# Optimization experiments

Measured on AMD Instinct MI355X. Metric: run time of the kernel, lower is better.

Reference implementation:

```python
import jax, jax.numpy as jnp
import numpy as np
from jax import lax

B, BERT_DIM, Z_DIM, ODE_UNITS, T_MAX = 4096, 768, 64, 128, 512
LN_EPS = 1e-5

def _glorot(key, shape):
    fan_in, fan_out = shape[0], shape[1]
    lim = float(np.sqrt(6.0 / (fan_in + fan_out)))
    return jax.random.uniform(key, shape, jnp.float32, -lim, lim)

def setup_inputs() -> dict:
    key = jax.random.key(0)
    ks = jax.random.split(key, 16)
    inp = {
        'bert_emb': jax.random.normal(ks[0], (B, BERT_DIM), jnp.float32),
        'times': jax.random.uniform(ks[1], (B, T_MAX), jnp.float32),
        'seq_lens': jax.random.randint(ks[2], (B,), 0, T_MAX).astype(jnp.int64),
        'eps': jax.random.normal(ks[3], (B, Z_DIM), jnp.float32),
        # bert_proj: Linear(768->64) + LayerNorm(64)
        'proj_W': _glorot(ks[4], (BERT_DIM, Z_DIM)),
        'proj_b': jnp.zeros((Z_DIM,), jnp.float32),
        'ln_g': jnp.ones((Z_DIM,), jnp.float32),
        'ln_b': jnp.zeros((Z_DIM,), jnp.float32),
        # DiffusionAug
        'log_noise_std': jnp.float32(-2.0),
        'den_W1': _glorot(ks[5], (Z_DIM, 2 * Z_DIM)),
        'den_b1': jnp.zeros((2 * Z_DIM,), jnp.float32),
        'den_W2': _glorot(ks[6], (2 * Z_DIM, Z_DIM)),
        'den_b2': jnp.zeros((Z_DIM,), jnp.float32),
        # ODEFunc: Linear->Tanh->Linear->Tanh->Linear (xavier_uniform, zero bias)
        'ode_W1': _glorot(ks[7], (Z_DIM, ODE_UNITS)),
        'ode_b1': jnp.zeros((ODE_UNITS,), jnp.float32),
        'ode_W2': _glorot(ks[8], (ODE_UNITS, ODE_UNITS)),
        'ode_b2': jnp.zeros((ODE_UNITS,), jnp.float32),
        'ode_W3': _glorot(ks[9], (ODE_UNITS, Z_DIM)),
        'ode_b3': jnp.zeros((Z_DIM,), jnp.float32),
        # dec_head: Linear(64->2)
        'dec_W': _glorot(ks[10], (Z_DIM, 2)),
        'dec_b': jnp.zeros((2,), jnp.float32),
    }
    return inp

def reference(bert_emb, times, seq_lens, eps, proj_W, proj_b, ln_g, ln_b,
              log_noise_std, den_W1, den_b1, den_W2, den_b2,
              ode_W1, ode_b1, ode_W2, ode_b2, ode_W3, ode_b3, dec_W, dec_b):
    T = times.shape[1]
    # bert_proj: Linear + LayerNorm (dropout = identity in eval)
    h = bert_emb @ proj_W + proj_b
    mu = jnp.mean(h, axis=-1, keepdims=True)
    var = jnp.var(h, axis=-1, keepdims=True)
    z_clean = (h - mu) * lax.rsqrt(var + LN_EPS) * ln_g + ln_b
    # DiffusionAug: noise + denoise MLP, MSE to detached clean latent
    sigma = jax.nn.softplus(log_noise_std)
    z_noisy = z_clean + sigma * eps
    z_aug = jax.nn.silu(z_noisy @ den_W1 + den_b1) @ den_W2 + den_b2
    diff_loss = jnp.mean((z_aug - lax.stop_gradient(z_clean)) ** 2)
    # Euler ODE integration: z <- z + dt * f(z), T sequential steps
    dt = jnp.float32(1.0 / max(T, 1))
    def step(z, _):
        f = jnp.tanh(jnp.tanh(z @ ode_W1 + ode_b1) @ ode_W2 + ode_b2) @ ode_W3 + ode_b3
        z_new = z + dt * f
        return z_new, z_new
    _, zs = lax.scan(step, z_aug, None, length=T)  # zs: (T, B, z)
    traj = jnp.concatenate([z_aug[:, None, :], jnp.swapaxes(zs, 0, 1)], axis=1)  # (B, T+1, z)
    out = traj @ dec_W + dec_b  # (B, T+1, 2)
    pred_delta = out[:, :, 0]
    stop_logits = out[:, :, 1]
    return (pred_delta, stop_logits, diff_loss)
```

## Files before the change

kernel.cpp:

```cpp
#include <hip/hip_runtime.h>
#include <stdint.h>

#define NB 4096
#define NT 512
#define OT 513
#define TOTE (NB*OT)
#define LOSSOFF (2*TOTE)

typedef float  f32x4 __attribute__((ext_vector_type(4)));
typedef __fp16 f16x8 __attribute__((ext_vector_type(8)));
typedef __fp16 f16x2 __attribute__((ext_vector_type(2)));

#define MFMA(A,B,C) __builtin_amdgcn_mfma_f32_16x16x32_f16((A),(B),(C),0,0,0)

__device__ __forceinline__ void wg_barrier() {
  asm volatile("s_waitcnt lgkmcnt(0)\n\ts_barrier" ::: "memory");
}

__device__ __forceinline__ float fast_tanh(float x) {
  float e = __builtin_amdgcn_exp2f(x * 2.8853900817779268f);
  return __builtin_fmaf(-2.0f, __builtin_amdgcn_rcpf(1.0f + e), 1.0f);
}
__device__ __forceinline__ float fast_silu(float x) {
  float e = __builtin_amdgcn_exp2f(x * -1.4426950408889634f);
  return x * __builtin_amdgcn_rcpf(1.0f + e);
}
__device__ __forceinline__ uint32_t pk2(float a, float b) {
  union { f16x2 h; uint32_t u; } c;
  c.h = __builtin_amdgcn_cvt_pkrtz(a, b);
  return c.u;
}
__device__ __forceinline__ f16x8 pack8(f32x4 a, f32x4 b) {
  union { f16x8 v; f16x2 h[4]; } u;
  u.h[0] = __builtin_amdgcn_cvt_pkrtz(a.x, a.y);
  u.h[1] = __builtin_amdgcn_cvt_pkrtz(a.z, a.w);
  u.h[2] = __builtin_amdgcn_cvt_pkrtz(b.x, b.y);
  u.h[3] = __builtin_amdgcn_cvt_pkrtz(b.z, b.w);
  return u.v;
}

#define WS_WPAK (1u<<20)
#define WS_UBUF ((1u<<20) + (256u<<10))
#define WS_CBUF ((1u<<20) + (384u<<10))

__global__ void compose_kernel(const float* __restrict__ oW1, const float* __restrict__ oW3,
                               const float* __restrict__ ob3, const float* __restrict__ dW,
                               float* __restrict__ Ubuf, float* __restrict__ cbuf,
                               float* __restrict__ dout) {
  int g = blockIdx.x, tid = threadIdx.x;
  if (g < 72) {
    int e = g * 256 + tid;
    int i = e / 144, j = e - i * 144;
    float s = 0.f;
    if (j < 128) {
      #pragma unroll 4
      for (int k = 0; k < 64; k++) s = __builtin_fmaf(oW3[i * 64 + k], oW1[k * 128 + j], s);
    } else if (j < 130) {
      int cc = j - 128;
      for (int k = 0; k < 64; k++) s = __builtin_fmaf(oW3[i * 64 + k], dW[k * 2 + cc], s);
    }
    Ubuf[i * 144 + j] = s;
  } else {
    if (tid < 144) {
      float s = 0.f;
      if (tid < 128) {
        for (int k = 0; k < 64; k++) s = __builtin_fmaf(ob3[k], oW1[k * 128 + tid], s);
      } else if (tid < 130) {
        int cc = tid - 128;
        for (int k = 0; k < 64; k++) s = __builtin_fmaf(ob3[k], dW[k * 2 + cc], s);
      }
      cbuf[tid] = s;
    }
    if (tid == 255) dout[LOSSOFF] = 0.0f;
  }
}

__global__ void pack_kernel(const float* __restrict__ oW1, const float* __restrict__ oW2,
                            const float* __restrict__ dW,  const float* __restrict__ dW1,
                            const float* __restrict__ dW2, const float* __restrict__ pW,
                            const float* __restrict__ Ubuf, char* __restrict__ wdst) {
  int g = blockIdx.x * 256 + threadIdx.x;
  int fid = g >> 6, lane = g & 63;
  if (fid >= 228 || (fid >= 50 && fid < 64)) return;
  int m4 = lane & 15;
  if (fid >= 48 && fid < 50) {
    int kt = fid - 48;
    int k0 = kt * 32 + (lane >> 4) * 8;
    f16x8 out;
    #pragma unroll
    for (int j = 0; j < 8; j++) out[j] = (m4 < 2) ? (__fp16)dW[(k0 + j) * 2 + m4] : (__fp16)0.f;
    *(f16x8*)(wdst + (size_t)(fid * 64 + lane) * 16) = out;
    return;
  }
  const float* src; int Kt, M, base;
  if      (fid < 16)  { src = oW1;  Kt = 2;  M = 128; base = 0;   }
  else if (fid < 48)  { src = oW2;  Kt = 4;  M = 128; base = 16;  }
  else if (fid < 80)  { src = dW1;  Kt = 2;  M = 128; base = 64;  }
  else if (fid < 96)  { src = dW2;  Kt = 4;  M = 64;  base = 80;  }
  else if (fid < 192) { src = pW;   Kt = 24; M = 64;  base = 96;  }
  else                { src = Ubuf; Kt = 4;  M = 144; base = 192; }
  int local = fid - base;
  int mt = local / Kt, kt = local % Kt;
  int m  = mt * 16 + m4;
  int k0 = kt * 32 + (lane >> 4) * 8;
  f16x8 out;
  #pragma unroll
  for (int j = 0; j < 8; j++) out[j] = (__fp16)src[(size_t)(k0 + j) * M + m];
  *(f16x8*)(wdst + (size_t)(fid * 64 + lane) * 16) = out;
}

__global__ __launch_bounds__(512, 2) void prologue_kernel(
    const float* __restrict__ bert, const float* __restrict__ eps,
    const float* __restrict__ projb, const float* __restrict__ lng,
    const float* __restrict__ lnb,  const float* __restrict__ lns,
    const float* __restrict__ db1,  const float* __restrict__ db2,
    const char* __restrict__ wpack, float* __restrict__ wsz,
    float* __restrict__ dout) {
  __shared__ __attribute__((aligned(16))) char sZ[16 * 128];
  __shared__ __attribute__((aligned(16))) char sH[16 * 256];
  __shared__ f32x4  sScr[4 * 64];
  __shared__ float2 sMV[64];
  __shared__ float  sLsum[4];

  const int tid  = threadIdx.x;
  const int wave = tid >> 6, lane = tid & 63;
  const int q = lane >> 4, b = lane & 15;
  const int bg = blockIdx.x * 16 + b;
  const int b7 = b & 7;
  const f16x8* wp = (const f16x8*)wpack;
  const int u0 = wave * 16 + q * 4;

  const int zr0 = b * 128 + ((q    ) ^ b7) * 16;
  const int zr1 = b * 128 + ((q + 4) ^ b7) * 16;
  int hr[4];
  #pragma unroll
  for (int s = 0; s < 4; s++) hr[s] = b * 256 + ((4 * s + q) ^ b7) * 16;
  const int hw = b * 256 + (((2 * wave + (q >> 1)) ^ b7) * 16) + (q & 1) * 8;
  const int zw = b * 128 + (((2 * (wave & 3) + (q >> 1)) ^ b7) * 16) + (q & 1) * 8;

  const int mt = wave & 3, kh = wave >> 2;
  f32x4 hA = {0,0,0,0}, hB = {0,0,0,0};
  #pragma unroll 4
  for (int i = 0; i < 12; i++) {
    int kt = kh * 12 + i;
    f16x8 af = wp[(size_t)(96 + mt * 24 + kt) * 64 + lane];
    const float* bp = bert + (size_t)bg * 768 + kt * 32 + q * 8;
    f32x4 f0 = *(const f32x4*)bp;
    f32x4 f1 = *(const f32x4*)(bp + 4);
    f16x8 bf = pack8(f0, f1);
    if (i & 1) hB = MFMA(af, bf, hB); else hA = MFMA(af, bf, hA);
  }
  f32x4 hacc = hA + hB;
  if (wave >= 4) sScr[(wave - 4) * 64 + lane] = hacc;
  __syncthreads();

  f32x4 h = {0,0,0,0}, zc = {0,0,0,0};
  if (wave < 4) {
    h = hacc + sScr[wave * 64 + lane];
    h.x += projb[u0 + 0]; h.y += projb[u0 + 1];
    h.z += projb[u0 + 2]; h.w += projb[u0 + 3];
    float s1 = h.x + h.y + h.z + h.w;
    float s2 = h.x*h.x + h.y*h.y + h.z*h.z + h.w*h.w;
    s1 += __shfl_xor(s1, 16); s1 += __shfl_xor(s1, 32);
    s2 += __shfl_xor(s2, 16); s2 += __shfl_xor(s2, 32);
    if (q == 0) sMV[wave * 16 + b] = make_float2(s1, s2);
  }
  __syncthreads();
  if (wave < 4) {
    float t1 = 0.f, t2 = 0.f;
    #pragma unroll
    for (int w2 = 0; w2 < 4; w2++) { float2 m = sMV[w2 * 16 + b]; t1 += m.x; t2 += m.y; }
    float mu  = t1 * (1.0f / 64.0f);
    float var = t2 * (1.0f / 64.0f) - mu * mu;
    float rs  = rsqrtf(var + 1e-5f);
    float sigma = logf(1.0f + expf(lns[0]));
    f32x4 e = *(const f32x4*)(eps + (size_t)bg * 64 + u0);
    zc.x = __builtin_fmaf((h.x - mu) * rs, lng[u0+0], lnb[u0+0]);
    zc.y = __builtin_fmaf((h.y - mu) * rs, lng[u0+1], lnb[u0+1]);
    zc.z = __builtin_fmaf((h.z - mu) * rs, lng[u0+2], lnb[u0+2]);
    zc.w = __builtin_fmaf((h.w - mu) * rs, lng[u0+3], lnb[u0+3]);
    f32x4 zn = zc + sigma * e;
    *(uint2*)(sZ + zw) = make_uint2(pk2(zn.x, zn.y), pk2(zn.z, zn.w));
  }
  __syncthreads();
  {
    f16x8 w0 = wp[(size_t)(64 + wave * 2 + 0) * 64 + lane];
    f16x8 w1 = wp[(size_t)(64 + wave * 2 + 1) * 64 + lane];
    f16x8 bz0 = *(const f16x8*)(sZ + zr0);
    f16x8 bz1 = *(const f16x8*)(sZ + zr1);
    f32x4 bias = { db1[u0+0], db1[u0+1], db1[u0+2], db1[u0+3] };
    f32x4 acc = MFMA(w0, bz0, bias);
    acc = MFMA(w1, bz1, acc);
    *(uint2*)(sH + hw) = make_uint2(pk2(fast_silu(acc.x), fast_silu(acc.y)),
                                    pk2(fast_silu(acc.z), fast_silu(acc.w)));
  }
  __syncthreads();
  if (wave < 4) {
    f16x8 w0 = wp[(size_t)(80 + wave * 4 + 0) * 64 + lane];
    f16x8 w1 = wp[(size_t)(80 + wave * 4 + 1) * 64 + lane];
    f16x8 w2 = wp[(size_t)(80 + wave * 4 + 2) * 64 + lane];
    f16x8 w3 = wp[(size_t)(80 + wave * 4 + 3) * 64 + lane];
    f16x8 g0 = *(const f16x8*)(sH + hr[0]);
    f16x8 g1 = *(const f16x8*)(sH + hr[1]);
    f16x8 g2 = *(const f16x8*)(sH + hr[2]);
    f16x8 g3 = *(const f16x8*)(sH + hr[3]);
    f32x4 bias = { db2[u0+0], db2[u0+1], db2[u0+2], db2[u0+3] };
    const f32x4 z4 = {0,0,0,0};
    f32x4 aA = MFMA(w0, g0, bias); aA = MFMA(w1, g1, aA);
    f32x4 aB = MFMA(w2, g2, z4);   aB = MFMA(w3, g3, aB);
    f32x4 za = aA + aB;
    *(f32x4*)(wsz + (size_t)bg * 64 + u0) = za;
    f32x4 d = za - zc;
    float sl = d.x*d.x + d.y*d.y + d.z*d.z + d.w*d.w;
    const int offs[6] = {1, 2, 4, 8, 16, 32};
    #pragma unroll
    for (int i = 0; i < 6; i++) sl += __shfl_xor(sl, offs[i]);
    if (lane == 0) sLsum[wave] = sl;
  }
  __syncthreads();
  if (tid == 0)
    atomicAdd(dout + LOSSOFF,
              (sLsum[0] + sLsum[1] + sLsum[2] + sLsum[3]) * (1.0f / 262144.0f));
}

__global__ __launch_bounds__(512, 1) void ode_kernel(
    const float* __restrict__ wsz, const char* __restrict__ wpack,
    const float* __restrict__ ob1, const float* __restrict__ cbuf,
    const float* __restrict__ ob2, const float* __restrict__ decb,
    float* __restrict__ dout) {
  __shared__ __attribute__((aligned(16))) char sH1[4096];
  __shared__ __attribute__((aligned(16))) char sH2[4096];

  const int tid  = threadIdx.x;
  const int wave = tid >> 6, lane = tid & 63;
  const int q = lane >> 4, b = lane & 15;
  const f16x8* wp = (const f16x8*)wpack;
  const float dtc = 1.0f / 512.0f;
  const f32x4 zero4 = {0,0,0,0};

  int rd[4];
  #pragma unroll
  for (int kt = 0; kt < 4; kt++) rd[kt] = b * 256 + (((kt * 4 + q) ^ b) * 16);
  const int wr = b * 256 + (((wave * 2 + (q >> 1)) ^ b) * 16) + (q & 1) * 8;

  f16x8 w2f[4], uf[4], uf8[4];
  #pragma unroll
  for (int kt = 0; kt < 4; kt++) {
    w2f[kt] = wp[(size_t)(16  + wave * 4 + kt) * 64 + lane];
    uf [kt] = wp[(size_t)(192 + wave * 4 + kt) * 64 + lane];
  }
  if (wave == 7) {
    #pragma unroll
    for (int kt = 0; kt < 4; kt++)
      uf8[kt] = wp[(size_t)(192 + 32 + kt) * 64 + lane];
  }
  const f32x4 b2f = *(const f32x4*)(ob2  + wave * 16 + q * 4);
  const f32x4 cw  = *(const f32x4*)(cbuf + wave * 16 + q * 4);
  const f32x4 c8  = *(const f32x4*)(cbuf + 128 + q * 4);

  const int bg = blockIdx.x * 16 + b;
  const float* zrow = wsz + (size_t)bg * 64;
  f32x4 z0a = *(const f32x4*)(zrow + q * 8);
  f32x4 z0b = *(const f32x4*)(zrow + q * 8 + 4);
  f32x4 z1a = *(const f32x4*)(zrow + 32 + q * 8);
  f32x4 z1b = *(const f32x4*)(zrow + 32 + q * 8 + 4);
  f16x8 zf0 = pack8(z0a, z0b);
  f16x8 zf1 = pack8(z1a, z1b);

  f32x4 b1v = *(const f32x4*)(ob1 + wave * 16 + q * 4);
  f32x4 G = MFMA(wp[(size_t)(wave * 2 + 0) * 64 + lane], zf0, b1v);
  G = MFMA(wp[(size_t)(wave * 2 + 1) * 64 + lane], zf1, G);
  *(uint2*)(sH1 + wr) = make_uint2(pk2(fast_tanh(G.x), fast_tanh(G.y)),
                                   pk2(fast_tanh(G.z), fast_tanh(G.w)));

  f32x4 Gd = zero4;
  float* const outp_p = dout + (size_t)bg * OT;
  float* const outp_s = dout + (size_t)TOTE + (size_t)bg * OT;
  if (wave == 7) {
    f32x4 b1d = zero4;
    if (q == 0) { b1d.x = decb[0]; b1d.y = decb[1]; }
    Gd = MFMA(wp[(size_t)48 * 64 + lane], zf0, b1d);
    Gd = MFMA(wp[(size_t)49 * 64 + lane], zf1, Gd);
    if (q == 0) { outp_p[0] = Gd.x; outp_s[0] = Gd.y; }
  }
  wg_barrier();

  #pragma unroll 1
  for (int t = 0; t < NT; ++t) {
    f16x8 p0 = *(const f16x8*)(sH1 + rd[0]);
    f16x8 p1 = *(const f16x8*)(sH1 + rd[1]);
    f16x8 p2 = *(const f16x8*)(sH1 + rd[2]);
    f16x8 p3 = *(const f16x8*)(sH1 + rd[3]);
    f32x4 a  = MFMA(w2f[0], p0, b2f);
    a  = MFMA(w2f[1], p1, a);
    f32x4 a2 = MFMA(w2f[2], p2, zero4);
    a2 = MFMA(w2f[3], p3, a2);
    f32x4 hv = a + a2;
    *(uint2*)(sH2 + wr) = make_uint2(pk2(fast_tanh(hv.x), fast_tanh(hv.y)),
                                     pk2(fast_tanh(hv.z), fast_tanh(hv.w)));
    wg_barrier();

    f16x8 g0 = *(const f16x8*)(sH2 + rd[0]);
    f16x8 g1 = *(const f16x8*)(sH2 + rd[1]);
    f16x8 g2 = *(const f16x8*)(sH2 + rd[2]);
    f16x8 g3 = *(const f16x8*)(sH2 + rd[3]);
    f32x4 d  = MFMA(uf[0], g0, cw);
    d  = MFMA(uf[1], g1, d);
    f32x4 d2 = MFMA(uf[2], g2, zero4);
    d2 = MFMA(uf[3], g3, d2);
    G.x = __builtin_fmaf(dtc, d.x + d2.x, G.x);
    G.y = __builtin_fmaf(dtc, d.y + d2.y, G.y);
    G.z = __builtin_fmaf(dtc, d.z + d2.z, G.z);
    G.w = __builtin_fmaf(dtc, d.w + d2.w, G.w);
    *(uint2*)(sH1 + wr) = make_uint2(pk2(fast_tanh(G.x), fast_tanh(G.y)),
                                     pk2(fast_tanh(G.z), fast_tanh(G.w)));
    if (wave == 7) {
      f32x4 e  = MFMA(uf8[0], g0, c8);
      e  = MFMA(uf8[1], g1, e);
      f32x4 e2 = MFMA(uf8[2], g2, zero4);
      e2 = MFMA(uf8[3], g3, e2);
      Gd.x = __builtin_fmaf(dtc, e.x + e2.x, Gd.x);
      Gd.y = __builtin_fmaf(dtc, e.y + e2.y, Gd.y);
      if (q == 0) { outp_p[t + 1] = Gd.x; outp_s[t + 1] = Gd.y; }
    }
    wg_barrier();
  }
}

extern "C" void kernel_launch(void* const* d_in, const int* in_sizes, int n_in,
                              void* d_out, int out_size, void* d_ws, size_t ws_size,
                              hipStream_t stream) {
  const float* bert  = (const float*)d_in[0];
  const float* eps   = (const float*)d_in[3];
  const float* projW = (const float*)d_in[4];
  const float* projb = (const float*)d_in[5];
  const float* lng   = (const float*)d_in[6];
  const float* lnb   = (const float*)d_in[7];
  const float* lns   = (const float*)d_in[8];
  const float* denW1 = (const float*)d_in[9];
  const float* denb1 = (const float*)d_in[10];
  const float* denW2 = (const float*)d_in[11];
  const float* denb2 = (const float*)d_in[12];
  const float* odeW1 = (const float*)d_in[13];
  const float* odeb1 = (const float*)d_in[14];
  const float* odeW2 = (const float*)d_in[15];
  const float* odeb2 = (const float*)d_in[16];
  const float* odeW3 = (const float*)d_in[17];
  const float* odeb3 = (const float*)d_in[18];
  const float* decW  = (const float*)d_in[19];
  const float* decb  = (const float*)d_in[20];
  float* dout = (float*)d_out;

  float* wsz  = (float*)d_ws;
  char*  wpak = (char*)d_ws + WS_WPAK;
  float* Ubuf = (float*)((char*)d_ws + WS_UBUF);
  float* cbuf = (float*)((char*)d_ws + WS_CBUF);

  compose_kernel<<<73, 256, 0, stream>>>(odeW1, odeW3, odeb3, decW, Ubuf, cbuf, dout);
  pack_kernel<<<57, 256, 0, stream>>>(odeW1, odeW2, decW, denW1, denW2, projW, Ubuf, wpak);
  prologue_kernel<<<256, 512, 0, stream>>>(bert, eps, projb, lng, lnb, lns,
                                           denb1, denb2, wpak, wsz, dout);
  ode_kernel<<<256, 512, 0, stream>>>(wsz, wpak, odeb1, cbuf, odeb2, decb, dout);
}
```

Before: 428.6 us.

## Halve ODE workgroup to 4 waves with two tiles each and stage outputs in LDS

The ODE kernel now runs 256 threads per block, and each wave computes two 16-row output tiles per layer, interleaving their MFMAs for more instruction-level parallelism. This cuts the number of waves that meet at each per-step barrier, which should lower sync cost in the serial 512-step loop. Decoder outputs are buffered in a 64KB LDS array during the loop and written to global memory coalesced at the end, replacing scattered per-step 4-byte stores. In exchange there is more register pressure per wave, fewer waves to hide latency, and a serialized epilogue store pass.

```diff
diff --git a/kernel.cpp b/kernel.cpp
--- a/kernel.cpp
+++ b/kernel.cpp
@@ -223,13 +223,14 @@
               (sLsum[0] + sLsum[1] + sLsum[2] + sLsum[3]) * (1.0f / 262144.0f));
 }
 
-__global__ __launch_bounds__(512, 1) void ode_kernel(
+__global__ __launch_bounds__(256, 1) void ode_kernel(
     const float* __restrict__ wsz, const char* __restrict__ wpack,
     const float* __restrict__ ob1, const float* __restrict__ cbuf,
     const float* __restrict__ ob2, const float* __restrict__ decb,
     float* __restrict__ dout) {
   __shared__ __attribute__((aligned(16))) char sH1[4096];
   __shared__ __attribute__((aligned(16))) char sH2[4096];
+  __shared__ __attribute__((aligned(16))) char sOut[65536];
 
   const int tid  = threadIdx.x;
   const int wave = tid >> 6, lane = tid & 63;
@@ -241,22 +242,36 @@
   int rd[4];
   #pragma unroll
   for (int kt = 0; kt < 4; kt++) rd[kt] = b * 256 + (((kt * 4 + q) ^ b) * 16);
-  const int wr = b * 256 + (((wave * 2 + (q >> 1)) ^ b) * 16) + (q & 1) * 8;
-
-  f16x8 w2f[4], uf[4], uf8[4];
-  #pragma unroll
-  for (int kt = 0; kt < 4; kt++) {
-    w2f[kt] = wp[(size_t)(16  + wave * 4 + kt) * 64 + lane];
-    uf [kt] = wp[(size_t)(192 + wave * 4 + kt) * 64 + lane];
-  }
-  if (wave == 7) {
+  int wr[2];
+  #pragma unroll
+  for (int s = 0; s < 2; s++) {
+    int T = wave + 4 * s;
+    wr[s] = b * 256 + (((T * 2 + (q >> 1)) ^ b) * 16) + (q & 1) * 8;
+  }
+
+  f16x8 w2f[2][4], uf[2][4], uf8[4];
+  #pragma unroll
+  for (int s = 0; s < 2; s++) {
+    int T = wave + 4 * s;
+    #pragma unroll
+    for (int kt = 0; kt < 4; kt++) {
+      w2f[s][kt] = wp[(size_t)(16  + T * 4 + kt) * 64 + lane];
+      uf [s][kt] = wp[(size_t)(192 + T * 4 + kt) * 64 + lane];
+    }
+  }
+  if (wave == 3) {
     #pragma unroll
     for (int kt = 0; kt < 4; kt++)
       uf8[kt] = wp[(size_t)(192 + 32 + kt) * 64 + lane];
   }
-  const f32x4 b2f = *(const f32x4*)(ob2  + wave * 16 + q * 4);
-  const f32x4 cw  = *(const f32x4*)(cbuf + wave * 16 + q * 4);
-  const f32x4 c8  = *(const f32x4*)(cbuf + 128 + q * 4);
+  f32x4 b2f[2], cw[2];
+  #pragma unroll
+  for (int s = 0; s < 2; s++) {
+    int T = wave + 4 * s;
+    b2f[s] = *(const f32x4*)(ob2  + T * 16 + q * 4);
+    cw [s] = *(const f32x4*)(cbuf + T * 16 + q * 4);
+  }
+  const f32x4 c8 = *(const f32x4*)(cbuf + 128 + q * 4);
 
   const int bg = blockIdx.x * 16 + b;
   const float* zrow = wsz + (size_t)bg * 64;
@@ -267,21 +282,27 @@
   f16x8 zf0 = pack8(z0a, z0b);
   f16x8 zf1 = pack8(z1a, z1b);
 
-  f32x4 b1v = *(const f32x4*)(ob1 + wave * 16 + q * 4);
-  f32x4 G = MFMA(wp[(size_t)(wave * 2 + 0) * 64 + lane], zf0, b1v);
-  G = MFMA(wp[(size_t)(wave * 2 + 1) * 64 + lane], zf1, G);
-  *(uint2*)(sH1 + wr) = make_uint2(pk2(fast_tanh(G.x), fast_tanh(G.y)),
-                                   pk2(fast_tanh(G.z), fast_tanh(G.w)));
+  f32x4 G[2];
+  #pragma unroll
+  for (int s = 0; s < 2; s++) {
+    int T = wave + 4 * s;
+    f32x4 b1v = *(const f32x4*)(ob1 + T * 16 + q * 4);
+    G[s] = MFMA(wp[(size_t)(T * 2 + 0) * 64 + lane], zf0, b1v);
+    G[s] = MFMA(wp[(size_t)(T * 2 + 1) * 64 + lane], zf1, G[s]);
+    *(uint2*)(sH1 + wr[s]) = make_uint2(pk2(fast_tanh(G[s].x), fast_tanh(G[s].y)),
+                                        pk2(fast_tanh(G[s].z), fast_tanh(G[s].w)));
+  }
 
   f32x4 Gd = zero4;
-  float* const outp_p = dout + (size_t)bg * OT;
-  float* const outp_s = dout + (size_t)TOTE + (size_t)bg * OT;
-  if (wave == 7) {
+  if (wave == 3) {
     f32x4 b1d = zero4;
     if (q == 0) { b1d.x = decb[0]; b1d.y = decb[1]; }
     Gd = MFMA(wp[(size_t)48 * 64 + lane], zf0, b1d);
     Gd = MFMA(wp[(size_t)49 * 64 + lane], zf1, Gd);
-    if (q == 0) { outp_p[0] = Gd.x; outp_s[0] = Gd.y; }
+    if (q == 0) {
+      dout[(size_t)bg * OT] = Gd.x;
+      dout[(size_t)TOTE + (size_t)bg * OT] = Gd.y;
+    }
   }
   wg_barrier();
 
@@ -291,39 +312,70 @@
     f16x8 p1 = *(const f16x8*)(sH1 + rd[1]);
     f16x8 p2 = *(const f16x8*)(sH1 + rd[2]);
     f16x8 p3 = *(const f16x8*)(sH1 + rd[3]);
-    f32x4 a  = MFMA(w2f[0], p0, b2f);
-    a  = MFMA(w2f[1], p1, a);
-    f32x4 a2 = MFMA(w2f[2], p2, zero4);
-    a2 = MFMA(w2f[3], p3, a2);
-    f32x4 hv = a + a2;
-    *(uint2*)(sH2 + wr) = make_uint2(pk2(fast_tanh(hv.x), fast_tanh(hv.y)),
-                                     pk2(fast_tanh(hv.z), fast_tanh(hv.w)));
+    f32x4 A[2], B[2];
+    A[0] = MFMA(w2f[0][0], p0, b2f[0]);
+    A[1] = MFMA(w2f[1][0], p0, b2f[1]);
+    A[0] = MFMA(w2f[0][1], p1, A[0]);
+    A[1] = MFMA(w2f[1][1], p1, A[1]);
+    B[0] = MFMA(w2f[0][2], p2, zero4);
+    B[1] = MFMA(w2f[1][2], p2, zero4);
+    B[0] = MFMA(w2f[0][3], p3, B[0]);
+    B[1] = MFMA(w2f[1][3], p3, B[1]);
+    #pragma unroll
+    for (int s = 0; s < 2; s++) {
+      f32x4 hv = A[s] + B[s];
+      *(uint2*)(sH2 + wr[s]) = make_uint2(pk2(fast_tanh(hv.x), fast_tanh(hv.y)),
+                                          pk2(fast_tanh(hv.z), fast_tanh(hv.w)));
+    }
     wg_barrier();
 
     f16x8 g0 = *(const f16x8*)(sH2 + rd[0]);
     f16x8 g1 = *(const f16x8*)(sH2 + rd[1]);
     f16x8 g2 = *(const f16x8*)(sH2 + rd[2]);
     f16x8 g3 = *(const f16x8*)(sH2 + rd[3]);
-    f32x4 d  = MFMA(uf[0], g0, cw);
-    d  = MFMA(uf[1], g1, d);
-    f32x4 d2 = MFMA(uf[2], g2, zero4);
-    d2 = MFMA(uf[3], g3, d2);
-    G.x = __builtin_fmaf(dtc, d.x + d2.x, G.x);
-    G.y = __builtin_fmaf(dtc, d.y + d2.y, G.y);
-    G.z = __builtin_fmaf(dtc, d.z + d2.z, G.z);
-    G.w = __builtin_fmaf(dtc, d.w + d2.w, G.w);
-    *(uint2*)(sH1 + wr) = make_uint2(pk2(fast_tanh(G.x), fast_tanh(G.y)),
-                                     pk2(fast_tanh(G.z), fast_tanh(G.w)));
-    if (wave == 7) {
+    f32x4 D[2], E[2];
+    D[0] = MFMA(uf[0][0], g0, cw[0]);
+    D[1] = MFMA(uf[1][0], g0, cw[1]);
+    D[0] = MFMA(uf[0][1], g1, D[0]);
+    D[1] = MFMA(uf[1][1], g1, D[1]);
+    E[0] = MFMA(uf[0][2], g2, zero4);
+    E[1] = MFMA(uf[1][2], g2, zero4);
+    E[0] = MFMA(uf[0][3], g3, E[0]);
+    E[1] = MFMA(uf[1][3], g3, E[1]);
+    #pragma unroll
+    for (int s = 0; s < 2; s++) {
+      f32x4 d = D[s] + E[s];
+      G[s].x = __builtin_fmaf(dtc, d.x, G[s].x);
+      G[s].y = __builtin_fmaf(dtc, d.y, G[s].y);
+      G[s].z = __builtin_fmaf(dtc, d.z, G[s].z);
+      G[s].w = __builtin_fmaf(dtc, d.w, G[s].w);
+      *(uint2*)(sH1 + wr[s]) = make_uint2(pk2(fast_tanh(G[s].x), fast_tanh(G[s].y)),
+                                          pk2(fast_tanh(G[s].z), fast_tanh(G[s].w)));
+    }
+    if (wave == 3) {
       f32x4 e  = MFMA(uf8[0], g0, c8);
       e  = MFMA(uf8[1], g1, e);
       f32x4 e2 = MFMA(uf8[2], g2, zero4);
       e2 = MFMA(uf8[3], g3, e2);
       Gd.x = __builtin_fmaf(dtc, e.x + e2.x, Gd.x);
       Gd.y = __builtin_fmaf(dtc, e.y + e2.y, Gd.y);
-      if (q == 0) { outp_p[t + 1] = Gd.x; outp_s[t + 1] = Gd.y; }
+      if (q == 0)
+        *(float2*)(sOut + b * 4096 + ((t ^ b) * 8)) = make_float2(Gd.x, Gd.y);
     }
     wg_barrier();
+  }
+
+  __syncthreads();
+  const int bg0 = blockIdx.x * 16;
+  #pragma unroll 1
+  for (int rb = 0; rb < 16; rb++) {
+    #pragma unroll
+    for (int h = 0; h < 2; h++) {
+      int t = h * 256 + tid;
+      float2 v = *(const float2*)(sOut + rb * 4096 + ((t ^ rb) * 8));
+      dout[(size_t)(bg0 + rb) * OT + 1 + t] = v.x;
+      dout[(size_t)TOTE + (size_t)(bg0 + rb) * OT + 1 + t] = v.y;
+    }
   }
 }
 
@@ -360,5 +412,5 @@
   pack_kernel<<<57, 256, 0, stream>>>(odeW1, odeW2, decW, denW1, denW2, projW, Ubuf, wpak);
   prologue_kernel<<<256, 512, 0, stream>>>(bert, eps, projb, lng, lnb, lns,
                                            denb1, denb2, wpak, wsz, dout);
-  ode_kernel<<<256, 512, 0, stream>>>(wsz, wpak, odeb1, cbuf, odeb2, decb, dout);
-}
+  ode_kernel<<<256, 256, 0, stream>>>(wsz, wpak, odeb1, cbuf, odeb2, decb, dout);
+}
```

New measurement: 492.9 us. 1.15x slower.
